# Kernel optimization log

Measured on AMD Instinct MI355X. Metric: run time of the kernel, lower is better.

## Reference

```python
import jax, jax.numpy as jnp
import numpy as np
from jax import lax

B, N, C = 4, 3072, 512
SAMPLE_RATIO = 0.25
CLUSTER_NUM = int(np.ceil(N * SAMPLE_RATIO))  # 768, static (mask=None, no 'r')
K = 5  # self.k, since k <= cluster_num


def setup_inputs() -> dict:
    key = jax.random.key(0)
    k1, = jax.random.split(key, 1)
    x = jax.random.normal(k1, (B, N, C), dtype=jnp.float32)
    # idx_token starts as identity mapping per batch (standard TCFormer init)
    idx_token = jnp.tile(jnp.arange(N, dtype=jnp.int32)[None, :], (B, 1))
    agg_weight = jnp.ones((B, N, 1), dtype=jnp.float32)
    return {"x": x, "idx_token": idx_token, "agg_weight": agg_weight}


def _cluster_dpc_knn(x):
    # runs under no_grad in torch -> stop_gradient here
    xs = lax.stop_gradient(x).astype(jnp.float32)
    sq = jnp.sum(xs * xs, axis=-1)  # [B,N]
    d2 = sq[:, :, None] + sq[:, None, :] - 2.0 * jnp.einsum('bnc,bmc->bnm', xs, xs)
    dist = jnp.sqrt(jnp.maximum(d2, 0.0)) / jnp.sqrt(jnp.float32(C))  # cdist / C**0.5
    # k nearest (smallest) distances
    neg_nearest, _ = lax.top_k(-dist, K)
    dist_nearest = -neg_nearest  # [B,N,K]
    density = jnp.exp(-jnp.mean(dist_nearest ** 2, axis=-1))
    density = density + jax.random.uniform(jax.random.key(42), density.shape, dtype=density.dtype) * 1e-6
    mask = (density[:, None, :] > density[:, :, None]).astype(x.dtype)  # [B,N,N]
    dist_max = jnp.max(dist.reshape(B, -1), axis=-1)[:, None, None]
    dist_min = jnp.min(dist * mask + dist_max * (1.0 - mask), axis=-1)  # [B,N]
    score = dist_min * density
    _, index_down = lax.top_k(score, CLUSTER_NUM)  # [B,cluster]
    # gather rows of dist at cluster centers, assign each token to nearest center
    dmat = jnp.take_along_axis(dist, index_down[:, :, None], axis=1)  # [B,cluster,N]
    idx_cluster = jnp.argmin(dmat, axis=1).astype(jnp.int32)  # [B,N]
    # force centers to map to their own cluster id
    idx_cluster = idx_cluster.at[jnp.arange(B)[:, None], index_down].set(
        jnp.broadcast_to(jnp.arange(CLUSTER_NUM, dtype=jnp.int32)[None, :], (B, CLUSTER_NUM)))
    return idx_cluster


def reference(x, idx_token, agg_weight):
    idx_cluster = _cluster_dpc_knn(x)
    # merge_tokens
    token_weight = jnp.ones((B, N, 1), dtype=x.dtype)
    idx = idx_cluster + jnp.arange(B, dtype=jnp.int32)[:, None] * CLUSTER_NUM  # [B,N]
    idx_flat = idx.reshape(-1)
    all_weight = jax.ops.segment_sum(token_weight.reshape(-1), idx_flat,
                                     num_segments=B * CLUSTER_NUM) + 1e-6  # [B*cluster]
    norm_weight = token_weight / all_weight[idx_flat].reshape(B, N, 1)  # [B,N,1]
    x_merged = jax.ops.segment_sum((x * norm_weight).reshape(B * N, C), idx_flat,
                                   num_segments=B * CLUSTER_NUM).reshape(B, CLUSTER_NUM, C)
    idx_token_new = jnp.take_along_axis(idx_cluster, idx_token, axis=1)  # [B,N]
    weight_t = jnp.take_along_axis(norm_weight, idx_token[:, :, None], axis=1)  # [B,N,1]
    agg_weight_new = agg_weight * weight_t
    return x_merged, agg_weight_new, idx_token_new, idx_cluster
```

## Files before the change

### kernel.cpp

```cpp
#include <hip/hip_runtime.h>
#include <math.h>
#include <float.h>

constexpr int B  = 4;
constexpr int N  = 3072;
constexpr int C  = 512;
constexpr int CL = 768;

typedef unsigned short u16;
typedef __attribute__((ext_vector_type(8))) short s16x8;
typedef __attribute__((ext_vector_type(4))) float f32x4;

__device__ __forceinline__ unsigned rotl32(unsigned v, int d) { return (v << d) | (v >> (32 - d)); }

__device__ inline void threefry2x32(unsigned k0, unsigned k1, unsigned c0, unsigned c1,
                                    unsigned& o0, unsigned& o1) {
  unsigned ks0 = k0, ks1 = k1, ks2 = 0x1BD11BDAu ^ k0 ^ k1;
  unsigned x0 = c0 + ks0, x1 = c1 + ks1;
#define TF_RND(r) { x0 += x1; x1 = rotl32(x1, (r)); x1 ^= x0; }
  TF_RND(13) TF_RND(15) TF_RND(26) TF_RND(6)  x0 += ks1; x1 += ks2 + 1u;
  TF_RND(17) TF_RND(29) TF_RND(16) TF_RND(24) x0 += ks2; x1 += ks0 + 2u;
  TF_RND(13) TF_RND(15) TF_RND(26) TF_RND(6)  x0 += ks0; x1 += ks1 + 3u;
  TF_RND(17) TF_RND(29) TF_RND(16) TF_RND(24) x0 += ks1; x1 += ks2 + 4u;
  TF_RND(13) TF_RND(15) TF_RND(26) TF_RND(6)  x0 += ks2; x1 += ks0 + 5u;
#undef TF_RND
  o0 = x0; o1 = x1;
}

__device__ inline float jax_uniform_bn(int f) {
  constexpr int HALF = (B * N) / 2;
  unsigned o0, o1, bits;
  if (f < HALF) { threefry2x32(0u, 42u, (unsigned)f, (unsigned)(f + HALF), o0, o1); bits = o0; }
  else          { threefry2x32(0u, 42u, (unsigned)(f - HALF), (unsigned)f, o0, o1); bits = o1; }
  return __uint_as_float((bits >> 9) | 0x3f800000u) - 1.0f;
}

__device__ __forceinline__ u16 bf16rn(float f) {
  unsigned u = __float_as_uint(f);
  unsigned r = u + 0x7FFFu + ((u >> 16) & 1u);
  return (u16)(r >> 16);
}
__device__ __forceinline__ float bf16tof(u16 h) {
  return __uint_as_float(((unsigned)h) << 16);
}

__global__ __launch_bounds__(64) void k_prep(const float* __restrict__ x, float* __restrict__ sq,
                                             u16* __restrict__ xhi, u16* __restrict__ xlo,
                                             int* __restrict__ counts,
                                             unsigned long long* __restrict__ packed,
                                             float* __restrict__ distmax) {
  int row = blockIdx.x;
  int lane = threadIdx.x;
  const float* xr = x + (size_t)row * C;
  u16* hr = xhi + (size_t)row * C;
  u16* lr = xlo + (size_t)row * C;
  float s = 0.f;
  for (int c = lane * 4; c < C; c += 256) {
    float4 v = *(const float4*)(xr + c);
    s += v.x * v.x + v.y * v.y + v.z * v.z + v.w * v.w;
    u16 h0 = bf16rn(v.x), h1 = bf16rn(v.y), h2 = bf16rn(v.z), h3 = bf16rn(v.w);
    u16 l0 = bf16rn(v.x - bf16tof(h0));
    u16 l1 = bf16rn(v.y - bf16tof(h1));
    u16 l2 = bf16rn(v.z - bf16tof(h2));
    u16 l3 = bf16rn(v.w - bf16tof(h3));
    uint2 hp, lp;
    hp.x = (unsigned)h0 | ((unsigned)h1 << 16); hp.y = (unsigned)h2 | ((unsigned)h3 << 16);
    lp.x = (unsigned)l0 | ((unsigned)l1 << 16); lp.y = (unsigned)l2 | ((unsigned)l3 << 16);
    *(uint2*)(hr + c) = hp;
    *(uint2*)(lr + c) = lp;
  }
  for (int o = 32; o > 0; o >>= 1) s += __shfl_down(s, o, 64);
  if (lane == 0) {
    sq[row] = s;
    packed[row] = ~0ull;
    if (row < B * CL) counts[row] = 0;
    if (row < B) distmax[row] = 0.f;
  }
}

__device__ __forceinline__ void ins5b(float t[5], float v) {
  float c = v;
  float n;
  n = fminf(t[0], c); c = fmaxf(t[0], c); t[0] = n;
  n = fminf(t[1], c); c = fmaxf(t[1], c); t[1] = n;
  n = fminf(t[2], c); c = fmaxf(t[2], c); t[2] = n;
  n = fminf(t[3], c); c = fmaxf(t[3], c); t[3] = n;
  t[4] = fminf(t[4], c);
}

constexpr int NT3 = N / 128;
constexpr int NTILE3 = NT3 * (NT3 + 1) / 2;

__global__ __launch_bounds__(256, 2) void k_distm(const u16* __restrict__ xhi, const u16* __restrict__ xlo,
                                                  const float* __restrict__ sq,
                                                  float* __restrict__ distbuf,
                                                  float* __restrict__ part5, int b0) {
  __shared__ __align__(16) char smem[65536];
  u16* smem_u16 = (u16*)smem;

  int bl = blockIdx.y, b = b0 + bl;

  int bx = blockIdx.x;
  constexpr int NX = 8, QX = NTILE3 / NX, RX = NTILE3 % NX;
  int xcd = bx % NX, sub = bx / NX;
  int idx = (xcd < RX ? xcd * (QX + 1) : RX * (QX + 1) + (xcd - RX) * QX) + sub;

  int ti = 0, rem = idx;
  while (rem >= NT3 - ti) { rem -= NT3 - ti; ++ti; }
  int tj = ti + rem;
  int i0 = ti * 128, j0 = tj * 128;
  bool do_mirror = (ti != tj);

  const float* sqb = sq + (size_t)b * N;
  float* dist = distbuf + (size_t)bl * N * N;

  int tid = threadIdx.x;
  int lane = tid & 63, w = tid >> 6;
  int wr = (w >> 1) * 64, wc = (w & 1) * 64;
  int l15 = lane & 15, l4 = lane >> 4;
  int csw = (lane >> 1) & 3;

  const u16* hil = (w & 1) ? xlo : xhi;
  int rbase0 = (w < 2) ? i0 : j0;
  const u16* gsrc = hil + ((size_t)b * N + rbase0 + (lane >> 2)) * C
                        + ((lane & 3) ^ ((lane >> 3) & 3)) * 8;

  f32x4 acc[4][4];
#pragma unroll
  for (int rt = 0; rt < 4; ++rt)
#pragma unroll
    for (int ct = 0; ct < 4; ++ct)
#pragma unroll
      for (int e = 0; e < 4; ++e) acc[rt][ct][e] = 0.f;

  {
    u16* lb = smem_u16 + w * 4096;
#pragma unroll
    for (int q = 0; q < 8; ++q)
      __builtin_amdgcn_global_load_lds(
          (const __attribute__((address_space(1))) void*)(gsrc + q * 16 * C),
          (__attribute__((address_space(3))) void*)(lb + q * 512), 16, 0, 0);
  }

#define KSTEP(CUR, STG, KNXT, DO_STAGE)                                              \
  {                                                                                  \
    if (DO_STAGE) {                                                                  \
      u16* lb = smem_u16 + (STG) * 16384 + w * 4096;                                 \
      const u16* gs = gsrc + (KNXT);                                                 \
      _Pragma("unroll")                                                              \
      for (int q = 0; q < 8; ++q)                                                    \
        __builtin_amdgcn_global_load_lds(                                            \
            (const __attribute__((address_space(1))) void*)(gs + q * 16 * C),        \
            (__attribute__((address_space(3))) void*)(lb + q * 512), 16, 0, 0);      \
      asm volatile("s_waitcnt vmcnt(8)" ::: "memory");                               \
    } else {                                                                         \
      asm volatile("s_waitcnt vmcnt(0)" ::: "memory");                               \
    }                                                                                \
    __builtin_amdgcn_s_barrier();                                                    \
    asm volatile("" ::: "memory");                                                   \
    const u16* sb = smem_u16 + (CUR) * 16384;                                        \
    s16x8 ah[4], al[4];                                                              \
    _Pragma("unroll")                                                                \
    for (int rt = 0; rt < 4; ++rt) {                                                 \
      int ro = (wr + rt * 16 + l15) * 32 + (l4 ^ csw) * 8;                           \
      ah[rt] = *(const s16x8*)(sb + ro);                                             \
      al[rt] = *(const s16x8*)(sb + 4096 + ro);                                      \
    }                                                                                \
    _Pragma("unroll")                                                                \
    for (int ct = 0; ct < 4; ++ct) {                                                 \
      int co = (wc + ct * 16 + l15) * 32 + (l4 ^ csw) * 8;                           \
      s16x8 bh = *(const s16x8*)(sb + 8192 + co);                                    \
      s16x8 bl = *(const s16x8*)(sb + 12288 + co);                                   \
      _Pragma("unroll")                                                              \
      for (int rt = 0; rt < 4; ++rt) {                                               \
        acc[rt][ct] = __builtin_amdgcn_mfma_f32_16x16x32_bf16(ah[rt], bh, acc[rt][ct], 0, 0, 0); \
        acc[rt][ct] = __builtin_amdgcn_mfma_f32_16x16x32_bf16(ah[rt], bl, acc[rt][ct], 0, 0, 0); \
        acc[rt][ct] = __builtin_amdgcn_mfma_f32_16x16x32_bf16(al[rt], bh, acc[rt][ct], 0, 0, 0); \
      }                                                                              \
    }                                                                                \
    asm volatile("" ::: "memory");                                                   \
    __builtin_amdgcn_s_barrier();                                                    \
    asm volatile("" ::: "memory");                                                   \
  }

  for (int ks = 0; ks < 16; ks += 2) {
    KSTEP(0, 1, (ks + 1) * 32, true)
    KSTEP(1, 0, (ks + 2) * 32, (ks + 2 < 16))
  }
#undef KSTEP

  const float SQC = 22.627416997969522f;
  float sqi[4][4], sqj[4];
#pragma unroll
  for (int rt = 0; rt < 4; ++rt)
#pragma unroll
    for (int r = 0; r < 4; ++r) sqi[rt][r] = sqb[i0 + wr + rt * 16 + l4 * 4 + r];
#pragma unroll
  for (int ct = 0; ct < 4; ++ct) sqj[ct] = sqb[j0 + wc + ct * 16 + l15];

#pragma unroll
  for (int rt = 0; rt < 4; ++rt)
#pragma unroll
    for (int ct = 0; ct < 4; ++ct)
#pragma unroll
      for (int r = 0; r < 4; ++r) {
        float d2 = fmaxf(sqi[rt][r] + sqj[ct] - 2.0f * acc[rt][ct][r], 0.0f);
        acc[rt][ct][r] = sqrtf(d2) / SQC;
      }

  constexpr int TSTR = 77;
  float* sT = (float*)smem + w * (32 * TSTR);

  float t5A[5] = {FLT_MAX, FLT_MAX, FLT_MAX, FLT_MAX, FLT_MAX};
  float mxA = 0.f;
  float4 dkeep[8];
  float t5B0[5] = {FLT_MAX, FLT_MAX, FLT_MAX, FLT_MAX, FLT_MAX};
  float mxB0 = 0.f;

#pragma unroll
  for (int p = 0; p < 2; ++p) {
#pragma unroll
    for (int cth = 0; cth < 2; ++cth) {
      int ct = p * 2 + cth;
      int cl = cth * 16 + l15;
#pragma unroll
      for (int rt = 0; rt < 4; ++rt)
#pragma unroll
        for (int r = 0; r < 4; ++r)
          sT[cl * TSTR + rt * 16 + l4 * 4 + r] = acc[rt][ct][r];
    }
    {
      int g4 = lane & 7, rbase = lane >> 3;
#pragma unroll
      for (int it = 0; it < 8; ++it) {
        int rl = it * 8 + rbase;
        float4 v = make_float4(sT[(4 * g4 + 0) * TSTR + rl],
                               sT[(4 * g4 + 1) * TSTR + rl],
                               sT[(4 * g4 + 2) * TSTR + rl],
                               sT[(4 * g4 + 3) * TSTR + rl]);
        if (p == 0) {
          dkeep[it] = v;
        } else {
          float* rp = dist + (size_t)(i0 + wr + rl) * N + j0 + wc;
          *(float4*)(rp + 4 * g4) = dkeep[it];
          *(float4*)(rp + 32 + 4 * g4) = v;
        }
      }
    }
    if (do_mirror) {
      int cg = lane >> 4, rq = lane & 15;
#pragma unroll
      for (int cc = 0; cc < 8; ++cc) {
        int c = cc * 4 + cg;
        float4 v;
        v.x = sT[c * TSTR + rq * 4 + 0];
        v.y = sT[c * TSTR + rq * 4 + 1];
        v.z = sT[c * TSTR + rq * 4 + 2];
        v.w = sT[c * TSTR + rq * 4 + 3];
        *(float4*)(dist + (size_t)(j0 + wc + p * 32 + c) * N + i0 + wr + rq * 4) = v;
      }
    }
    for (int c = 0; c < 32; ++c) {
      float v = sT[c * TSTR + lane];
      mxA = fmaxf(mxA, v);
      ins5b(t5A, v);
    }
    if (do_mirror) {
      int cl = lane & 31, half = lane >> 5;
      float t5B[5] = {FLT_MAX, FLT_MAX, FLT_MAX, FLT_MAX, FLT_MAX};
      float mxB = 0.f;
      for (int k = 0; k < 32; ++k) {
        float v = sT[cl * TSTR + half * 32 + k];
        mxB = fmaxf(mxB, v);
        ins5b(t5B, v);
      }
      mxB = fmaxf(mxB, __shfl_xor(mxB, 32, 64));
      float o0 = __shfl_xor(t5B[0], 32, 64);
      float o1 = __shfl_xor(t5B[1], 32, 64);
      float o2 = __shfl_xor(t5B[2], 32, 64);
      float o3 = __shfl_xor(t5B[3], 32, 64);
      float o4 = __shfl_xor(t5B[4], 32, 64);
      ins5b(t5B, o0); ins5b(t5B, o1); ins5b(t5B, o2); ins5b(t5B, o3); ins5b(t5B, o4);
      if (p == 0) {
        t5B0[0] = t5B[0]; t5B0[1] = t5B[1]; t5B0[2] = t5B[2];
        t5B0[3] = t5B[3]; t5B0[4] = t5B[4]; mxB0 = mxB;
      } else if (half == 0) {
        int slotB = ti * 2 + (wr >> 6);
        float* dst = part5 + (((size_t)bl * 48 + slotB) * 6) * N + (j0 + wc + cl);
        dst[0] = t5B0[0];                dst[32] = t5B[0];
        dst[(size_t)N] = t5B0[1];        dst[(size_t)N + 32] = t5B[1];
        dst[2 * (size_t)N] = t5B0[2];    dst[2 * (size_t)N + 32] = t5B[2];
        dst[3 * (size_t)N] = t5B0[3];    dst[3 * (size_t)N + 32] = t5B[3];
        dst[4 * (size_t)N] = t5B0[4];    dst[4 * (size_t)N + 32] = t5B[4];
        dst[5 * (size_t)N] = mxB0;       dst[5 * (size_t)N + 32] = mxB;
      }
    }
  }
  {
    int rowA = i0 + wr + lane;
    int slotA = tj * 2 + (wc >> 6);
    float* dst = part5 + (((size_t)bl * 48 + slotA) * 6) * N + rowA;
    dst[0] = t5A[0]; dst[(size_t)N] = t5A[1]; dst[2 * (size_t)N] = t5A[2];
    dst[3 * (size_t)N] = t5A[3]; dst[4 * (size_t)N] = t5A[4]; dst[5 * (size_t)N] = mxA;
  }
}

__global__ __launch_bounds__(256) void k_dens(const float* __restrict__ part5,
                                              float* __restrict__ density,
                                              float* __restrict__ distmax, int b0) {
  __shared__ float red[4][64][6];
  int tid = threadIdx.x;
  int rr = tid & 63, sg = tid >> 6;
  int row0 = blockIdx.x * 64;
  int bl = row0 / N, r = (row0 % N) + rr;
  int b = b0 + bl;
  const float* base = part5 + (size_t)bl * 48 * 6 * N + r;
  float t5[5] = {FLT_MAX, FLT_MAX, FLT_MAX, FLT_MAX, FLT_MAX};
  float mx = 0.f;
  for (int s = sg * 12; s < sg * 12 + 12; ++s) {
    const float* sp = base + (size_t)s * 6 * N;
    ins5b(t5, sp[0]);
    ins5b(t5, sp[(size_t)N]);
    ins5b(t5, sp[2 * (size_t)N]);
    ins5b(t5, sp[3 * (size_t)N]);
    ins5b(t5, sp[4 * (size_t)N]);
    mx = fmaxf(mx, sp[5 * (size_t)N]);
  }
  red[sg][rr][0] = t5[0]; red[sg][rr][1] = t5[1]; red[sg][rr][2] = t5[2];
  red[sg][rr][3] = t5[3]; red[sg][rr][4] = t5[4]; red[sg][rr][5] = mx;
  __syncthreads();
  if (sg == 0) {
#pragma unroll
    for (int g = 1; g < 4; ++g) {
      ins5b(t5, red[g][rr][0]);
      ins5b(t5, red[g][rr][1]);
      ins5b(t5, red[g][rr][2]);
      ins5b(t5, red[g][rr][3]);
      ins5b(t5, red[g][rr][4]);
      mx = fmaxf(mx, red[g][rr][5]);
    }
    float sum = t5[0] * t5[0] + t5[1] * t5[1] + t5[2] * t5[2] + t5[3] * t5[3] + t5[4] * t5[4];
    density[b * N + r] = expf(-(sum / 5.0f)) + jax_uniform_bn(b * N + r) * 1e-6f;
#pragma unroll
    for (int m = 1; m < 64; m <<= 1) mx = fmaxf(mx, __shfl_xor(mx, m, 64));
    if (rr == 0) atomicMax((int*)(distmax + b), __float_as_int(mx));
  }
}

__global__ __launch_bounds__(256) void k_maskmin(const float* __restrict__ distbuf,
                                                 const float* __restrict__ density,
                                                 const float* __restrict__ distmax,
                                                 float* __restrict__ score, int b0) {
  __shared__ float sd[N];
  int tid = threadIdx.x;
  int wv = tid >> 6, lane = tid & 63;
  int bl = blockIdx.y, b = b0 + bl;
  const float* db = density + (size_t)b * N;
  for (int j = tid * 4; j < N; j += 1024) *(float4*)(sd + j) = *(const float4*)(db + j);
  __syncthreads();
  int i0r = blockIdx.x * 16 + wv * 4;
  float dmax = distmax[b];
  const float* row0 = distbuf + ((size_t)bl * N + i0r) * N;
  float di0 = sd[i0r], di1 = sd[i0r + 1], di2 = sd[i0r + 2], di3 = sd[i0r + 3];
  float mn0 = dmax, mn1 = dmax, mn2 = dmax, mn3 = dmax;
#pragma unroll 2
  for (int it = 0; it < N / 256; ++it) {
    int j = it * 256 + lane * 4;
    float4 d  = *(const float4*)(sd + j);
    float4 v0 = *(const float4*)(row0 + j);
    float4 v1 = *(const float4*)(row0 + (size_t)N + j);
    float4 v2 = *(const float4*)(row0 + 2 * (size_t)N + j);
    float4 v3 = *(const float4*)(row0 + 3 * (size_t)N + j);
    mn0 = fminf(mn0, (d.x > di0) ? v0.x : dmax);
    mn0 = fminf(mn0, (d.y > di0) ? v0.y : dmax);
    mn0 = fminf(mn0, (d.z > di0) ? v0.z : dmax);
    mn0 = fminf(mn0, (d.w > di0) ? v0.w : dmax);
    mn1 = fminf(mn1, (d.x > di1) ? v1.x : dmax);
    mn1 = fminf(mn1, (d.y > di1) ? v1.y : dmax);
    mn1 = fminf(mn1, (d.z > di1) ? v1.z : dmax);
    mn1 = fminf(mn1, (d.w > di1) ? v1.w : dmax);
    mn2 = fminf(mn2, (d.x > di2) ? v2.x : dmax);
    mn2 = fminf(mn2, (d.y > di2) ? v2.y : dmax);
    mn2 = fminf(mn2, (d.z > di2) ? v2.z : dmax);
    mn2 = fminf(mn2, (d.w > di2) ? v2.w : dmax);
    mn3 = fminf(mn3, (d.x > di3) ? v3.x : dmax);
    mn3 = fminf(mn3, (d.y > di3) ? v3.y : dmax);
    mn3 = fminf(mn3, (d.z > di3) ? v3.z : dmax);
    mn3 = fminf(mn3, (d.w > di3) ? v3.w : dmax);
  }
#pragma unroll
  for (int m = 1; m < 64; m <<= 1) {
    mn0 = fminf(mn0, __shfl_xor(mn0, m, 64));
    mn1 = fminf(mn1, __shfl_xor(mn1, m, 64));
    mn2 = fminf(mn2, __shfl_xor(mn2, m, 64));
    mn3 = fminf(mn3, __shfl_xor(mn3, m, 64));
  }
  if (lane == 0) {
    score[b * N + i0r]     = mn0 * di0;
    score[b * N + i0r + 1] = mn1 * di1;
    score[b * N + i0r + 2] = mn2 * di2;
    score[b * N + i0r + 3] = mn3 * di3;
  }
}

__global__ __launch_bounds__(256) void k_rank(const float* __restrict__ score,
                                              int* __restrict__ index_down,
                                              int* __restrict__ rank, int b0) {
  __shared__ float ssc[N];
  int tid = threadIdx.x;
  int wv = tid >> 6, lane = tid & 63;
  int b = b0 + blockIdx.y;
  const float* sb = score + (size_t)b * N;
  for (int j = tid * 4; j < N; j += 1024) *(float4*)(ssc + j) = *(const float4*)(sb + j);
  __syncthreads();
  int i0r = blockIdx.x * 16 + wv * 4;
  float s0 = ssc[i0r], s1 = ssc[i0r + 1], s2 = ssc[i0r + 2], s3 = ssc[i0r + 3];
  int c0 = 0, c1 = 0, c2 = 0, c3 = 0;
#pragma unroll 2
  for (int it = 0; it < N / 256; ++it) {
    int j = it * 256 + lane * 4;
    float4 v = *(const float4*)(ssc + j);
    c0 += (v.x > s0) || (v.x == s0 && (j + 0) < i0r);
    c0 += (v.y > s0) || (v.y == s0 && (j + 1) < i0r);
    c0 += (v.z > s0) || (v.z == s0 && (j + 2) < i0r);
    c0 += (v.w > s0) || (v.w == s0 && (j + 3) < i0r);
    c1 += (v.x > s1) || (v.x == s1 && (j + 0) < i0r + 1);
    c1 += (v.y > s1) || (v.y == s1 && (j + 1) < i0r + 1);
    c1 += (v.z > s1) || (v.z == s1 && (j + 2) < i0r + 1);
    c1 += (v.w > s1) || (v.w == s1 && (j + 3) < i0r + 1);
    c2 += (v.x > s2) || (v.x == s2 && (j + 0) < i0r + 2);
    c2 += (v.y > s2) || (v.y == s2 && (j + 1) < i0r + 2);
    c2 += (v.z > s2) || (v.z == s2 && (j + 2) < i0r + 2);
    c2 += (v.w > s2) || (v.w == s2 && (j + 3) < i0r + 2);
    c3 += (v.x > s3) || (v.x == s3 && (j + 0) < i0r + 3);
    c3 += (v.y > s3) || (v.y == s3 && (j + 1) < i0r + 3);
    c3 += (v.z > s3) || (v.z == s3 && (j + 2) < i0r + 3);
    c3 += (v.w > s3) || (v.w == s3 && (j + 3) < i0r + 3);
  }
#pragma unroll
  for (int m = 1; m < 64; m <<= 1) {
    c0 += __shfl_xor(c0, m, 64);
    c1 += __shfl_xor(c1, m, 64);
    c2 += __shfl_xor(c2, m, 64);
    c3 += __shfl_xor(c3, m, 64);
  }
  if (lane == 0) {
    rank[b * N + i0r]     = (c0 < CL) ? c0 : -1;
    rank[b * N + i0r + 1] = (c1 < CL) ? c1 : -1;
    rank[b * N + i0r + 2] = (c2 < CL) ? c2 : -1;
    rank[b * N + i0r + 3] = (c3 < CL) ? c3 : -1;
    if (c0 < CL) index_down[b * CL + c0] = i0r;
    if (c1 < CL) index_down[b * CL + c1] = i0r + 1;
    if (c2 < CL) index_down[b * CL + c2] = i0r + 2;
    if (c3 < CL) index_down[b * CL + c3] = i0r + 3;
  }
}

__global__ __launch_bounds__(256) void k_assign_part(const float* __restrict__ distbuf,
                                                     const int* __restrict__ index_down,
                                                     unsigned long long* __restrict__ packed, int b0) {
  constexpr int RCH = CL / 8;
  __shared__ int sid[RCH];
  int bl = blockIdx.z, b = b0 + bl;
  int r0 = blockIdx.y * RCH;
  int tid = threadIdx.x;
  for (int r = tid; r < RCH; r += 256) sid[r] = index_down[b * CL + r0 + r];
  __syncthreads();
  int j = blockIdx.x * 256 + tid;
  const float* base = distbuf + (size_t)bl * N * N;
  float best = FLT_MAX; int bestr = 0;
#pragma unroll 8
  for (int r = 0; r < RCH; ++r) {
    float d = base[(size_t)sid[r] * N + j];
    if (d < best) { best = d; bestr = r0 + r; }
  }
  unsigned long long key = ((unsigned long long)__float_as_uint(best) << 32) | (unsigned)bestr;
  atomicMin(&packed[b * N + j], key);
}

__global__ void k_assign_fin2(const unsigned long long* __restrict__ packed,
                              const int* __restrict__ rank,
                              int* __restrict__ idx_cluster, int* __restrict__ counts) {
  int g = blockIdx.x * 256 + threadIdx.x;
  int b = g / N;
  int r = rank[g];
  int cl = (r >= 0) ? r : (int)(unsigned)(packed[g] & 0xffffffffull);
  idx_cluster[g] = cl;
  atomicAdd(&counts[b * CL + cl], 1);
}

__global__ __launch_bounds__(1024) void k_scan(const int* __restrict__ counts,
                                               int* __restrict__ offsets, int* __restrict__ cursor) {
  constexpr int T = B * CL;
  __shared__ int sm[T];
  int tid = threadIdx.x;
  for (int p = tid; p < T; p += 1024) sm[p] = counts[p];
  __syncthreads();
  for (int off = 1; off < T; off <<= 1) {
    int v[3]; int n = 0;
    for (int p = tid; p < T; p += 1024) { v[n++] = (p >= off) ? sm[p - off] : 0; }
    __syncthreads();
    n = 0;
    for (int p = tid; p < T; p += 1024) { sm[p] += v[n++]; }
    __syncthreads();
  }
  for (int p = tid; p < T; p += 1024) {
    int e = sm[p] - counts[p];
    offsets[p] = e; cursor[p] = e;
  }
}

__global__ void k_fill(const int* __restrict__ idx_cluster, int* __restrict__ cursor,
                       int* __restrict__ members) {
  int g = blockIdx.x * 256 + threadIdx.x;
  int b = g / N, i = g % N;
  int seg = b * CL + idx_cluster[g];
  int pos = atomicAdd(&cursor[seg], 1);
  members[pos] = i;
}

__global__ __launch_bounds__(128) void k_gather(const float* __restrict__ x, const int* __restrict__ members,
                                                const int* __restrict__ offsets, const int* __restrict__ counts,
                                                float* __restrict__ out0) {
  int seg = blockIdx.x;
  int b = seg / CL;
  int cnt = counts[seg], off = offsets[seg];
  float nw = 1.0f / ((float)cnt + 1e-6f);
  int c = threadIdx.x * 4;
  const float* xb = x + (size_t)b * N * C;
  float4 acc = make_float4(0.f, 0.f, 0.f, 0.f);
  for (int m = 0; m < cnt; ++m) {
    int tok = members[off + m];
    float4 v = *(const float4*)(xb + (size_t)tok * C + c);
    acc.x += v.x * nw; acc.y += v.y * nw; acc.z += v.z * nw; acc.w += v.w * nw;
  }
  *(float4*)(out0 + (size_t)seg * C + c) = acc;
}

__global__ void k_final(const float* __restrict__ agg_weight, const int* __restrict__ idx_token,
                        const int* __restrict__ idx_cluster, const int* __restrict__ counts,
                        float* __restrict__ out1, float* __restrict__ out2, float* __restrict__ out3) {
  int g = blockIdx.x * 256 + threadIdx.x;
  int b = g / N;
  int it = idx_token[g];
  int clt = idx_cluster[b * N + it];
  float nwt = 1.0f / ((float)counts[b * CL + clt] + 1e-6f);
  out1[g] = agg_weight[g] * nwt;
  out2[g] = (float)clt;
  out3[g] = (float)idx_cluster[g];
}

extern "C" void kernel_launch(void* const* d_in, const int* in_sizes, int n_in,
                              void* d_out, int out_size, void* d_ws, size_t ws_size,
                              hipStream_t stream) {
  const float* x          = (const float*)d_in[0];
  const int*   idx_token  = (const int*)d_in[1];
  const float* agg_weight = (const float*)d_in[2];

  float* out0 = (float*)d_out;
  float* out1 = out0 + (size_t)B * CL * C;
  float* out2 = out1 + (size_t)B * N;
  float* out3 = out2 + (size_t)B * N;

  char* w = (char*)d_ws;
  auto carve = [&](size_t bytes) { char* p = w; w += (bytes + 255) & ~(size_t)255; return p; };
  float*    sq         = (float*)carve((size_t)B * N * 4);
  float*    density    = (float*)carve((size_t)B * N * 4);
  float*    score      = (float*)carve((size_t)B * N * 4);
  float*    distmax    = (float*)carve((size_t)B * 4);
  int*      index_down = (int*)carve((size_t)B * CL * 4);
  int*      rank       = (int*)carve((size_t)B * N * 4);
  int*      idx_clus   = (int*)carve((size_t)B * N * 4);
  int*      counts     = (int*)carve((size_t)B * CL * 4);
  int*      offsets    = (int*)carve((size_t)B * CL * 4);
  int*      cursor     = (int*)carve((size_t)B * CL * 4);
  int*      members    = (int*)carve((size_t)B * N * 4);
  unsigned long long* packed = (unsigned long long*)carve((size_t)B * N * 8);
  u16*      xhi        = (u16*)carve((size_t)B * N * C * 2);
  u16*      xlo        = (u16*)carve((size_t)B * N * C * 2);
  float*    part5      = (float*)carve((size_t)B * 48 * 6 * N * 4);
  size_t used = (size_t)(w - (char*)d_ws);
  size_t per  = (size_t)N * N * 4;
  int nb_max = (ws_size > used) ? (int)((ws_size - used) / per) : 0;
  if (nb_max < 1) nb_max = 1;
  if (nb_max > B) nb_max = B;
  float* distbuf = (float*)w;

  k_prep<<<B * N, 64, 0, stream>>>(x, sq, xhi, xlo, counts, packed, distmax);

  for (int b0 = 0; b0 < B; b0 += nb_max) {
    int nb = (B - b0 < nb_max) ? (B - b0) : nb_max;
    k_distm<<<dim3(NTILE3, nb), 256, 0, stream>>>(xhi, xlo, sq, distbuf, part5, b0);
    k_dens<<<(nb * N) / 64, 256, 0, stream>>>(part5, density, distmax, b0);
    k_maskmin<<<dim3(N / 16, nb), 256, 0, stream>>>(distbuf, density, distmax, score, b0);
    k_rank<<<dim3(N / 16, nb), 256, 0, stream>>>(score, index_down, rank, b0);
    k_assign_part<<<dim3(N / 256, 8, nb), 256, 0, stream>>>(distbuf, index_down, packed, b0);
  }

  k_assign_fin2<<<(B * N) / 256, 256, 0, stream>>>(packed, rank, idx_clus, counts);
  k_scan<<<1, 1024, 0, stream>>>(counts, offsets, cursor);
  k_fill<<<(B * N) / 256, 256, 0, stream>>>(idx_clus, cursor, members);
  k_gather<<<B * CL, 128, 0, stream>>>(x, members, offsets, counts, out0);
  k_final<<<(B * N) / 256, 256, 0, stream>>>(agg_weight, idx_token, idx_clus, counts, out1, out2, out3);
}
```

Measured before the change: 278.8 us.

## Single-buffer LDS staging in distance GEMM to raise occupancy to four blocks

Replaces the double-buffered global-to-LDS pipeline in the distance-matrix GEMM kernel with a single buffer. Each k-step now loads, waits on vmcnt(0), computes, then reloads. LDS drops from 64KB to about 38.5KB and launch bounds go to 4 blocks per CU, so more waves can hide latency. The cost is that load/compute overlap inside a block is lost and there are extra barriers per step. The 4-block bound may also force register spills given the 64 accumulator floats per thread.

Measured after the change: 289.7 us. 1.04x slower.

```diff
diff --git a/kernel.cpp b/kernel.cpp
--- a/kernel.cpp
+++ b/kernel.cpp
@@ -91,11 +91,11 @@
 constexpr int NT3 = N / 128;
 constexpr int NTILE3 = NT3 * (NT3 + 1) / 2;
 
-__global__ __launch_bounds__(256, 2) void k_distm(const u16* __restrict__ xhi, const u16* __restrict__ xlo,
+__global__ __launch_bounds__(256, 4) void k_distm(const u16* __restrict__ xhi, const u16* __restrict__ xlo,
                                                   const float* __restrict__ sq,
                                                   float* __restrict__ distbuf,
                                                   float* __restrict__ part5, int b0) {
-  __shared__ __align__(16) char smem[65536];
+  __shared__ __align__(16) char smem[39424];
   u16* smem_u16 = (u16*)smem;
 
   int bl = blockIdx.y, b = b0 + bl;
@@ -124,6 +124,7 @@
   int rbase0 = (w < 2) ? i0 : j0;
   const u16* gsrc = hil + ((size_t)b * N + rbase0 + (lane >> 2)) * C
                         + ((lane & 3) ^ ((lane >> 3) & 3)) * 8;
+  u16* lb = smem_u16 + w * 4096;
 
   f32x4 acc[4][4];
 #pragma unroll
@@ -133,61 +134,52 @@
 #pragma unroll
       for (int e = 0; e < 4; ++e) acc[rt][ct][e] = 0.f;
 
-  {
-    u16* lb = smem_u16 + w * 4096;
-#pragma unroll
-    for (int q = 0; q < 8; ++q)
-      __builtin_amdgcn_global_load_lds(
-          (const __attribute__((address_space(1))) void*)(gsrc + q * 16 * C),
-          (__attribute__((address_space(3))) void*)(lb + q * 512), 16, 0, 0);
-  }
-
-#define KSTEP(CUR, STG, KNXT, DO_STAGE)                                              \
-  {                                                                                  \
-    if (DO_STAGE) {                                                                  \
-      u16* lb = smem_u16 + (STG) * 16384 + w * 4096;                                 \
-      const u16* gs = gsrc + (KNXT);                                                 \
-      _Pragma("unroll")                                                              \
-      for (int q = 0; q < 8; ++q)                                                    \
-        __builtin_amdgcn_global_load_lds(                                            \
-            (const __attribute__((address_space(1))) void*)(gs + q * 16 * C),        \
-            (__attribute__((address_space(3))) void*)(lb + q * 512), 16, 0, 0);      \
-      asm volatile("s_waitcnt vmcnt(8)" ::: "memory");                               \
-    } else {                                                                         \
-      asm volatile("s_waitcnt vmcnt(0)" ::: "memory");                               \
-    }                                                                                \
-    __builtin_amdgcn_s_barrier();                                                    \
-    asm volatile("" ::: "memory");                                                   \
-    const u16* sb = smem_u16 + (CUR) * 16384;                                        \
-    s16x8 ah[4], al[4];                                                              \
-    _Pragma("unroll")                                                                \
-    for (int rt = 0; rt < 4; ++rt) {                                                 \
-      int ro = (wr + rt * 16 + l15) * 32 + (l4 ^ csw) * 8;                           \
-      ah[rt] = *(const s16x8*)(sb + ro);                                             \
-      al[rt] = *(const s16x8*)(sb + 4096 + ro);                                      \
-    }                                                                                \
-    _Pragma("unroll")                                                                \
-    for (int ct = 0; ct < 4; ++ct) {                                                 \
-      int co = (wc + ct * 16 + l15) * 32 + (l4 ^ csw) * 8;                           \
-      s16x8 bh = *(const s16x8*)(sb + 8192 + co);                                    \
-      s16x8 bl = *(const s16x8*)(sb + 12288 + co);                                   \
-      _Pragma("unroll")                                                              \
-      for (int rt = 0; rt < 4; ++rt) {                                               \
-        acc[rt][ct] = __builtin_amdgcn_mfma_f32_16x16x32_bf16(ah[rt], bh, acc[rt][ct], 0, 0, 0); \
-        acc[rt][ct] = __builtin_amdgcn_mfma_f32_16x16x32_bf16(ah[rt], bl, acc[rt][ct], 0, 0, 0); \
-        acc[rt][ct] = __builtin_amdgcn_mfma_f32_16x16x32_bf16(al[rt], bh, acc[rt][ct], 0, 0, 0); \
-      }                                                                              \
-    }                                                                                \
-    asm volatile("" ::: "memory");                                                   \
-    __builtin_amdgcn_s_barrier();                                                    \
-    asm volatile("" ::: "memory");                                                   \
-  }
-
-  for (int ks = 0; ks < 16; ks += 2) {
-    KSTEP(0, 1, (ks + 1) * 32, true)
-    KSTEP(1, 0, (ks + 2) * 32, (ks + 2 < 16))
-  }
-#undef KSTEP
+#pragma unroll
+  for (int q = 0; q < 8; ++q)
+    __builtin_amdgcn_global_load_lds(
+        (const __attribute__((address_space(1))) void*)(gsrc + q * 16 * C),
+        (__attribute__((address_space(3))) void*)(lb + q * 512), 16, 0, 0);
+  asm volatile("s_waitcnt vmcnt(0)" ::: "memory");
+  __builtin_amdgcn_s_barrier();
+  asm volatile("" ::: "memory");
+
+#pragma unroll 2
+  for (int ks = 0; ks < 16; ++ks) {
+    const u16* sb = smem_u16;
+    s16x8 ah[4], al[4];
+#pragma unroll
+    for (int rt = 0; rt < 4; ++rt) {
+      int ro = (wr + rt * 16 + l15) * 32 + (l4 ^ csw) * 8;
+      ah[rt] = *(const s16x8*)(sb + ro);
+      al[rt] = *(const s16x8*)(sb + 4096 + ro);
+    }
+#pragma unroll
+    for (int ct = 0; ct < 4; ++ct) {
+      int co = (wc + ct * 16 + l15) * 32 + (l4 ^ csw) * 8;
+      s16x8 bh = *(const s16x8*)(sb + 8192 + co);
+      s16x8 bl = *(const s16x8*)(sb + 12288 + co);
+#pragma unroll
+      for (int rt = 0; rt < 4; ++rt) {
+        acc[rt][ct] = __builtin_amdgcn_mfma_f32_16x16x32_bf16(ah[rt], bh, acc[rt][ct], 0, 0, 0);
+        acc[rt][ct] = __builtin_amdgcn_mfma_f32_16x16x32_bf16(ah[rt], bl, acc[rt][ct], 0, 0, 0);
+        acc[rt][ct] = __builtin_amdgcn_mfma_f32_16x16x32_bf16(al[rt], bh, acc[rt][ct], 0, 0, 0);
+      }
+    }
+    asm volatile("s_waitcnt lgkmcnt(0)" ::: "memory");
+    __builtin_amdgcn_s_barrier();
+    asm volatile("" ::: "memory");
+    if (ks + 1 < 16) {
+      const u16* gs = gsrc + (ks + 1) * 32;
+#pragma unroll
+      for (int q = 0; q < 8; ++q)
+        __builtin_amdgcn_global_load_lds(
+            (const __attribute__((address_space(1))) void*)(gs + q * 16 * C),
+            (__attribute__((address_space(3))) void*)(lb + q * 512), 16, 0, 0);
+      asm volatile("s_waitcnt vmcnt(0)" ::: "memory");
+      __builtin_amdgcn_s_barrier();
+      asm volatile("" ::: "memory");
+    }
+  }
 
   const float SQC = 22.627416997969522f;
   float sqi[4][4], sqj[4];
```
